# Performance work log

Measured on AMD Instinct MI355X. Metric: run time of the kernel, lower is better.

The kernel has to match this reference:

```python
import jax, jax.numpy as jnp
import numpy as np

B, T, FEAT, FUSION, H, C = 128, 64, 4096, 1024, 1024, 2


def setup_inputs() -> dict:
    key = jax.random.key(0)
    ks = jax.random.split(key, 9)
    s_feat = 1.0 / np.sqrt(FEAT)
    s_h = 1.0 / np.sqrt(H)
    return {
        "x": jax.random.normal(ks[0], (B, T, FEAT), jnp.float32),
        "W_feat": jax.random.normal(ks[1], (FUSION, FEAT), jnp.float32) * s_feat,
        "b_feat": jax.random.normal(ks[2], (FUSION,), jnp.float32) * s_feat,
        "W_ih": jax.random.normal(ks[3], (4 * H, FUSION), jnp.float32) * s_h,
        "b_ih": jax.random.normal(ks[4], (4 * H,), jnp.float32) * s_h,
        "W_hh": jax.random.normal(ks[5], (4 * H, H), jnp.float32) * s_h,
        "b_hh": jax.random.normal(ks[6], (4 * H,), jnp.float32) * s_h,
        "W_cls": jax.random.normal(ks[7], (C, H), jnp.float32) * s_h,
        "b_cls": jax.random.normal(ks[8], (C,), jnp.float32) * s_h,
    }


def reference(x, W_feat, b_feat, W_ih, b_ih, W_hh, b_hh, W_cls, b_cls):
    # x: [B, T, FEAT]. Sequential LSTMCell loop expressed as lax.scan over time.
    Hdim = W_hh.shape[1]
    Bb = x.shape[0]
    h0 = jnp.zeros((Bb, Hdim), x.dtype)
    c0 = jnp.zeros((Bb, Hdim), x.dtype)

    def step(carry, x_t):
        h, c = carry
        # feature extractor: Linear + ReLU fusion (dropout = identity in eval)
        f = jax.nn.relu(x_t @ W_feat.T + b_feat)  # [B, FUSION]
        gates = f @ W_ih.T + b_ih + h @ W_hh.T + b_hh  # [B, 4H]
        i, fg, g, o = jnp.split(gates, 4, axis=-1)  # torch LSTMCell gate order
        i = jax.nn.sigmoid(i)
        fg = jax.nn.sigmoid(fg)
        g = jnp.tanh(g)
        o = jax.nn.sigmoid(o)
        c_new = fg * c + i * g
        h_new = o * jnp.tanh(c_new)
        s = h_new @ W_cls.T + b_cls  # [B, 2]
        return (h_new, c_new), s

    xs = jnp.swapaxes(x, 0, 1)  # [T, B, FEAT]
    _, scores = jax.lax.scan(step, (h0, c0), xs)  # [T, B, 2]
    return jnp.swapaxes(scores, 0, 1)  # [B, T, 2]
```

## Files before the change

### kernel.cpp

```cpp
#include <hip/hip_runtime.h>
#include <math.h>


typedef __attribute__((ext_vector_type(8))) short short8v;
typedef __attribute__((ext_vector_type(4))) float f32x4;
typedef unsigned short u16;

#define HF2_BUF 262144
#define HF2_MT  32768

__device__ __forceinline__ short f2h(float f) {
    return __builtin_bit_cast(short, (_Float16)f);
}
__device__ __forceinline__ float h2f(u16 h) {
    return (float)__builtin_bit_cast(_Float16, (short)h);
}

__global__ void cvt_f16(const float* __restrict__ src, u16* __restrict__ d, int n4) {
    int i = blockIdx.x * blockDim.x + threadIdx.x;
    if (i >= n4) return;
    float4 v = ((const float4*)src)[i];
    ushort4 o;
    o.x = (u16)f2h(v.x); o.y = (u16)f2h(v.y);
    o.z = (u16)f2h(v.z); o.w = (u16)f2h(v.w);
    ((ushort4*)d)[i] = o;
}

template<bool A_PRE16, bool RELU, bool OUT_F16, bool OUT_GI>
__global__ __launch_bounds__(256)
void gemm_f16(const float* __restrict__ Af,
              const u16* __restrict__ A16, int lda,
              const u16* __restrict__ B16, int ldb,
              const float* __restrict__ bias,
              float* __restrict__ C, u16* __restrict__ C16,
              int ldc, int K)
{
    __shared__ short8v As[8][64];
    __shared__ short8v Bs[8][64];

    const int tid = threadIdx.x;
    const int l   = tid & 63;
    const int w   = tid >> 6;
    const int wm  = w & 1, wn = w >> 1;
    const int bm  = blockIdx.x * 128, bn = blockIdx.y * 128;

    const int sm    = tid >> 2;
    const int sk8   = (tid & 3) * 8;
    const int koct_s = sk8 >> 3;
    const int slane = ((sm & 15) ^ (koct_s << 1)) | (koct_s << 4);
    const int smf   = sm >> 4;
    const int lsw   = ((l & 15) ^ ((l >> 4) << 1)) | (l & 48);

    f32x4 acc[4][4];
#pragma unroll
    for (int i = 0; i < 4; ++i)
#pragma unroll
        for (int j = 0; j < 4; ++j)
#pragma unroll
            for (int r = 0; r < 4; ++r) acc[i][j][r] = 0.f;

    for (int k0 = 0; k0 < K; k0 += 32) {
        if constexpr (A_PRE16) {
            const size_t o0 = (size_t)(bm + sm) * lda + k0 + sk8;
            const size_t o1 = (size_t)(bm + sm + 64) * lda + k0 + sk8;
            As[smf][slane]     = *(const short8v*)(A16 + o0);
            As[smf + 4][slane] = *(const short8v*)(A16 + o1);
        } else {
            float fa[8], fb[8];
            const float* p0 = Af + (size_t)(bm + sm) * lda + k0 + sk8;
            const float* p1 = Af + (size_t)(bm + sm + 64) * lda + k0 + sk8;
            *(float4*)(fa)     = *(const float4*)(p0);
            *(float4*)(fa + 4) = *(const float4*)(p0 + 4);
            *(float4*)(fb)     = *(const float4*)(p1);
            *(float4*)(fb + 4) = *(const float4*)(p1 + 4);
            short8v ha, hb;
#pragma unroll
            for (int e = 0; e < 8; ++e) { ha[e] = f2h(fa[e]); hb[e] = f2h(fb[e]); }
            As[smf][slane]     = ha;
            As[smf + 4][slane] = hb;
        }
        {
            const size_t o0 = (size_t)(bn + sm) * ldb + k0 + sk8;
            const size_t o1 = (size_t)(bn + sm + 64) * ldb + k0 + sk8;
            Bs[smf][slane]     = *(const short8v*)(B16 + o0);
            Bs[smf + 4][slane] = *(const short8v*)(B16 + o1);
        }
        __syncthreads();

        short8v a[4];
#pragma unroll
        for (int i = 0; i < 4; ++i) a[i] = As[wm * 4 + i][lsw];
#pragma unroll
        for (int j = 0; j < 4; ++j) {
            const short8v b = Bs[wn * 4 + j][lsw];
#pragma unroll
            for (int i = 0; i < 4; ++i)
                acc[i][j] = __builtin_amdgcn_mfma_f32_16x16x32_f16(a[i], b, acc[i][j], 0, 0, 0);
        }
        __syncthreads();
    }

    const int row0 = bm + wm * 64 + (l >> 4) * 4;
    const int col0 = bn + wn * 64 + (l & 15);
#pragma unroll
    for (int i = 0; i < 4; ++i) {
#pragma unroll
        for (int j = 0; j < 4; ++j) {
            const int col = col0 + j * 16;
            const float bs = bias[col];
#pragma unroll
            for (int r = 0; r < 4; ++r) {
                const int row = row0 + i * 16 + r;
                float v = acc[i][j][r] + bs;
                if (RELU) v = fmaxf(v, 0.f);
                if (OUT_F16) {
                    C16[(size_t)row * ldc + col] = (u16)f2h(v);
                } else if (OUT_GI) {
                    const size_t rr = (size_t)(row & 63) * 128 + (row >> 6);
                    C16[rr * 4096 + (size_t)(col & 1023) * 4 + (col >> 10)] = (u16)f2h(v);
                } else {
                    C[(size_t)row * ldc + col] = v;
                }
            }
        }
    }
}

__global__ void pack_whh3(const float* __restrict__ W, char* __restrict__ Wf) {
    int gid = blockIdx.x * blockDim.x + threadIdx.x;
    int l = gid & 63, fid = gid >> 6;
    int kcl = fid & 15, kh = (fid >> 4) & 1, ngrp = (fid >> 5) & 63, g = fid >> 11;
    int n = g * 1024 + ngrp * 16 + (l & 15);
    int k = kh * 512 + kcl * 32 + (l >> 4) * 8;
    const float* src = W + (size_t)n * 1024 + k;
    short8v v16;
#pragma unroll
    for (int e = 0; e < 8; ++e) v16[e] = f2h(src[e]);
    *(short8v*)(Wf + (size_t)fid * 1024 + (size_t)l * 16) = v16;
}

__global__ void out_init(float* __restrict__ out, const float* __restrict__ b_cls) {
    int i = blockIdx.x * blockDim.x + threadIdx.x;
    if (i < 16384) out[i] = b_cls[i & 1];
}

__global__ __launch_bounds__(512)
void lstm_step(const u16* __restrict__ Gxi,
               const float* __restrict__ b_hh,
               const char*  __restrict__ Wf,
               char*        __restrict__ hfrag,
               float*       __restrict__ c,
               const float* __restrict__ Wc,
               float*       __restrict__ out,
               int t)
{
    __shared__ short8v Hs[64][64];
    __shared__ float gates_s[2][4][32][16];
    __shared__ float h_s[32][16];
    __shared__ float Wc_s[2][16];

    const int tid = threadIdx.x, bid = blockIdx.x;
    const int w = tid >> 6, l = tid & 63;
    const int g = w & 3, kh = w >> 2;
    const int ngrp = bid & 63, mh = bid >> 6;

    if (tid < 32) Wc_s[tid >> 4][tid & 15] =
        Wc[(size_t)(tid >> 4) * 1024 + ngrp * 16 + (tid & 15)];

    const int lhi = l >> 4;
    const int llo = l & 15;

    f32x4 aE0, aO0, aE1, aO1;
#pragma unroll
    for (int r = 0; r < 4; ++r) { aE0[r] = 0.f; aO0[r] = 0.f; aE1[r] = 0.f; aO1[r] = 0.f; }

    if (t > 0) {
        const char* hbase = hfrag + ((t - 1) & 1) * HF2_BUF;
#pragma unroll
        for (int it = 0; it < 8; ++it) {
            const int u  = tid + it * 512;
            const int s  = u >> 6;
            const int ln = u & 63;
            Hs[s][ln] = *(const short8v*)(hbase
                        + (size_t)(2 * mh + (s >> 5)) * HF2_MT
                        + (size_t)(s & 31) * 1024 + (size_t)ln * 16);
        }
        __syncthreads();

        const char* wb = Wf + (size_t)((g * 64 + ngrp) * 2 + kh) * 16384 + (size_t)l * 16;
#pragma unroll
        for (int kcl = 0; kcl < 16; kcl += 2) {
            const short8v b0 = *(const short8v*)(wb + kcl * 1024);
            const short8v b1 = *(const short8v*)(wb + (kcl + 1) * 1024);
            const int kc0 = kh * 16 + kcl;
            aE0 = __builtin_amdgcn_mfma_f32_16x16x32_f16(Hs[kc0][l],      b0, aE0, 0, 0, 0);
            aE1 = __builtin_amdgcn_mfma_f32_16x16x32_f16(Hs[32 + kc0][l], b0, aE1, 0, 0, 0);
            aO0 = __builtin_amdgcn_mfma_f32_16x16x32_f16(Hs[kc0 + 1][l],      b1, aO0, 0, 0, 0);
            aO1 = __builtin_amdgcn_mfma_f32_16x16x32_f16(Hs[32 + kc0 + 1][l], b1, aO1, 0, 0, 0);
        }
    }

#pragma unroll
    for (int r = 0; r < 4; ++r) {
        gates_s[kh][g][lhi * 4 + r][llo]      = aE0[r] + aO0[r];
        gates_s[kh][g][16 + lhi * 4 + r][llo] = aE1[r] + aO1[r];
    }
    __syncthreads();

    {
        const int r  = tid >> 4;
        const int cw = tid & 15;
        const int row = mh * 32 + r;
        const int col = ngrp * 16 + cw;
        const ushort4 gv = *(const ushort4*)(Gxi
                          + ((size_t)t * 128 + row) * 4096 + (size_t)col * 4);
        float gate[4];
        gate[0] = h2f(gv.x); gate[1] = h2f(gv.y);
        gate[2] = h2f(gv.z); gate[3] = h2f(gv.w);
#pragma unroll
        for (int gg = 0; gg < 4; ++gg)
            gate[gg] += gates_s[0][gg][r][cw] + gates_s[1][gg][r][cw]
                      + b_hh[gg * 1024 + col];
        float ig = 1.f / (1.f + __expf(-gate[0]));
        float fg = 1.f / (1.f + __expf(-gate[1]));
        float gg = tanhf(gate[2]);
        float og = 1.f / (1.f + __expf(-gate[3]));
        const size_t cidx = (size_t)row * 1024 + col;
        float cp = (t > 0) ? c[cidx] : 0.f;
        float cn = fg * cp + ig * gg;
        float hn = og * tanhf(cn);
        c[cidx] = cn;
        h_s[r][cw] = hn;

        float s0 = hn * Wc_s[0][cw];
        float s1 = hn * Wc_s[1][cw];
#pragma unroll
        for (int off = 8; off > 0; off >>= 1) {
            s0 += __shfl_xor(s0, off);
            s1 += __shfl_xor(s1, off);
        }
        if (cw == 0) {
            float* o = out + ((size_t)row * 64 + t) * 2;
            atomicAdd(o,     s0);
            atomicAdd(o + 1, s1);
        }
    }
    __syncthreads();

    if (tid < 64) {
        const int idx16  = tid & 15;
        const int koct_h = (tid >> 4) & 1;
        const int mt_l   = (tid >> 5) & 1;
        const int lane   = idx16 | (((ngrp & 1) * 2 + koct_h) << 4);
        short8v v;
#pragma unroll
        for (int e = 0; e < 8; ++e)
            v[e] = f2h(h_s[mt_l * 16 + idx16][koct_h * 8 + e]);
        char* dst = hfrag + (t & 1) * HF2_BUF
                  + (size_t)(2 * mh + mt_l) * HF2_MT
                  + (size_t)(ngrp >> 1) * 1024 + (size_t)lane * 16;
        *(short8v*)dst = v;
    }
}

extern "C" void kernel_launch(void* const* d_in, const int* in_sizes, int n_in,
                              void* d_out, int out_size, void* d_ws, size_t ws_size,
                              hipStream_t stream) {
    const float* x      = (const float*)d_in[0];
    const float* W_feat = (const float*)d_in[1];
    const float* b_feat = (const float*)d_in[2];
    const float* W_ih   = (const float*)d_in[3];
    const float* b_ih   = (const float*)d_in[4];
    const float* W_hh   = (const float*)d_in[5];
    const float* b_hh   = (const float*)d_in[6];
    const float* W_cls  = (const float*)d_in[7];
    const float* b_cls  = (const float*)d_in[8];
    float* out = (float*)d_out;

    char* ws = (char*)d_ws;
    u16*  F16   = (u16*)ws;
    u16*  Wih16 = (u16*)(ws + 16777216);
    u16*  Wf16  = (u16*)(ws + 25165824);
    u16*  Gxi   = (u16*)(ws + 33554432);
    char* Wf    = ws;
    char* hfrag = ws + 16777216;
    float* c    = (float*)(ws + 17825792);

    cvt_f16<<<dim3(4096), dim3(256), 0, stream>>>(W_feat, Wf16, 1048576);
    cvt_f16<<<dim3(4096), dim3(256), 0, stream>>>(W_ih, Wih16, 1048576);
    out_init<<<dim3(64), dim3(256), 0, stream>>>(out, b_cls);

    gemm_f16<false, true, true, false>
        <<<dim3(64, 8), 256, 0, stream>>>(
            x, nullptr, 4096, Wf16, 4096, b_feat,
            nullptr, F16, 1024, 4096);

    gemm_f16<true, false, false, true>
        <<<dim3(64, 32), 256, 0, stream>>>(
            nullptr, F16, 1024, Wih16, 1024, b_ih,
            nullptr, Gxi, 4096, 1024);

    pack_whh3<<<dim3(2048), dim3(256), 0, stream>>>(W_hh, Wf);

    for (int t = 0; t < 64; ++t) {
        lstm_step<<<dim3(256), dim3(512), 0, stream>>>(
            Gxi, b_hh, Wf, hfrag, c, W_cls, out, t);
    }
}
```

Measured before the change: 725.3 us.

## Fold b_hh into GEMM bias, prefetch gate inputs early, widen BK for feature GEMM

Adds a small kernel that pre-sums b_ih and b_hh so the input-projection GEMM bakes both biases into Gxi. This removes the per-step b_hh loads in the recurrent kernel. The Gxi gate values and previous cell state are now loaded at the start of lstm_step, so their latency overlaps the recurrent MFMA work. The feature GEMM also gets a templated K-tile of 64, which halves the number of barriers per K and doubles the LDS footprint.

```diff
diff --git a/kernel.cpp b/kernel.cpp
--- a/kernel.cpp
+++ b/kernel.cpp
@@ -26,7 +26,13 @@
     ((ushort4*)d)[i] = o;
 }
 
-template<bool A_PRE16, bool RELU, bool OUT_F16, bool OUT_GI>
+__global__ void add_bias(const float* __restrict__ a, const float* __restrict__ b,
+                         float* __restrict__ o, int n) {
+    int i = blockIdx.x * blockDim.x + threadIdx.x;
+    if (i < n) o[i] = a[i] + b[i];
+}
+
+template<int BK, bool A_PRE16, bool RELU, bool OUT_F16, bool OUT_GI>
 __global__ __launch_bounds__(256)
 void gemm_f16(const float* __restrict__ Af,
               const u16* __restrict__ A16, int lda,
@@ -35,8 +41,9 @@
               float* __restrict__ C, u16* __restrict__ C16,
               int ldc, int K)
 {
-    __shared__ short8v As[8][64];
-    __shared__ short8v Bs[8][64];
+    constexpr int NH = BK / 32;
+    __shared__ short8v As[NH * 8][64];
+    __shared__ short8v Bs[NH * 8][64];
 
     const int tid = threadIdx.x;
     const int l   = tid & 63;
@@ -59,43 +66,44 @@
 #pragma unroll
             for (int r = 0; r < 4; ++r) acc[i][j][r] = 0.f;
 
-    for (int k0 = 0; k0 < K; k0 += 32) {
-        if constexpr (A_PRE16) {
-            const size_t o0 = (size_t)(bm + sm) * lda + k0 + sk8;
-            const size_t o1 = (size_t)(bm + sm + 64) * lda + k0 + sk8;
-            As[smf][slane]     = *(const short8v*)(A16 + o0);
-            As[smf + 4][slane] = *(const short8v*)(A16 + o1);
-        } else {
-            float fa[8], fb[8];
-            const float* p0 = Af + (size_t)(bm + sm) * lda + k0 + sk8;
-            const float* p1 = Af + (size_t)(bm + sm + 64) * lda + k0 + sk8;
-            *(float4*)(fa)     = *(const float4*)(p0);
-            *(float4*)(fa + 4) = *(const float4*)(p0 + 4);
-            *(float4*)(fb)     = *(const float4*)(p1);
-            *(float4*)(fb + 4) = *(const float4*)(p1 + 4);
-            short8v ha, hb;
-#pragma unroll
-            for (int e = 0; e < 8; ++e) { ha[e] = f2h(fa[e]); hb[e] = f2h(fb[e]); }
-            As[smf][slane]     = ha;
-            As[smf + 4][slane] = hb;
-        }
-        {
-            const size_t o0 = (size_t)(bn + sm) * ldb + k0 + sk8;
-            const size_t o1 = (size_t)(bn + sm + 64) * ldb + k0 + sk8;
-            Bs[smf][slane]     = *(const short8v*)(B16 + o0);
-            Bs[smf + 4][slane] = *(const short8v*)(B16 + o1);
+    for (int k0 = 0; k0 < K; k0 += BK) {
+#pragma unroll
+        for (int h = 0; h < NH; ++h) {
+            const int kk = k0 + h * 32 + sk8;
+            if constexpr (A_PRE16) {
+                As[h * 8 + smf][slane]     = *(const short8v*)(A16 + (size_t)(bm + sm) * lda + kk);
+                As[h * 8 + smf + 4][slane] = *(const short8v*)(A16 + (size_t)(bm + sm + 64) * lda + kk);
+            } else {
+                float fa[8], fb[8];
+                const float* p0 = Af + (size_t)(bm + sm) * lda + kk;
+                const float* p1 = Af + (size_t)(bm + sm + 64) * lda + kk;
+                *(float4*)(fa)     = *(const float4*)(p0);
+                *(float4*)(fa + 4) = *(const float4*)(p0 + 4);
+                *(float4*)(fb)     = *(const float4*)(p1);
+                *(float4*)(fb + 4) = *(const float4*)(p1 + 4);
+                short8v ha, hb;
+#pragma unroll
+                for (int e = 0; e < 8; ++e) { ha[e] = f2h(fa[e]); hb[e] = f2h(fb[e]); }
+                As[h * 8 + smf][slane]     = ha;
+                As[h * 8 + smf + 4][slane] = hb;
+            }
+            Bs[h * 8 + smf][slane]     = *(const short8v*)(B16 + (size_t)(bn + sm) * ldb + kk);
+            Bs[h * 8 + smf + 4][slane] = *(const short8v*)(B16 + (size_t)(bn + sm + 64) * ldb + kk);
         }
         __syncthreads();
 
-        short8v a[4];
-#pragma unroll
-        for (int i = 0; i < 4; ++i) a[i] = As[wm * 4 + i][lsw];
-#pragma unroll
-        for (int j = 0; j < 4; ++j) {
-            const short8v b = Bs[wn * 4 + j][lsw];
-#pragma unroll
-            for (int i = 0; i < 4; ++i)
-                acc[i][j] = __builtin_amdgcn_mfma_f32_16x16x32_f16(a[i], b, acc[i][j], 0, 0, 0);
+#pragma unroll
+        for (int h = 0; h < NH; ++h) {
+            short8v a[4];
+#pragma unroll
+            for (int i = 0; i < 4; ++i) a[i] = As[h * 8 + wm * 4 + i][lsw];
+#pragma unroll
+            for (int j = 0; j < 4; ++j) {
+                const short8v b = Bs[h * 8 + wn * 4 + j][lsw];
+#pragma unroll
+                for (int i = 0; i < 4; ++i)
+                    acc[i][j] = __builtin_amdgcn_mfma_f32_16x16x32_f16(a[i], b, acc[i][j], 0, 0, 0);
+            }
         }
         __syncthreads();
     }
@@ -146,7 +154,6 @@
 
 __global__ __launch_bounds__(512)
 void lstm_step(const u16* __restrict__ Gxi,
-               const float* __restrict__ b_hh,
                const char*  __restrict__ Wf,
                char*        __restrict__ hfrag,
                float*       __restrict__ c,
@@ -164,6 +171,15 @@
     const int g = w & 3, kh = w >> 2;
     const int ngrp = bid & 63, mh = bid >> 6;
 
+    const int r_c  = tid >> 4;
+    const int cw_c = tid & 15;
+    const int row_c = mh * 32 + r_c;
+    const int col_c = ngrp * 16 + cw_c;
+    const ushort4 gv = *(const ushort4*)(Gxi
+                      + ((size_t)t * 128 + row_c) * 4096 + (size_t)col_c * 4);
+    const size_t cidx = (size_t)row_c * 1024 + col_c;
+    const float cp = (t > 0) ? c[cidx] : 0.f;
+
     if (tid < 32) Wc_s[tid >> 4][tid & 15] =
         Wc[(size_t)(tid >> 4) * 1024 + ngrp * 16 + (tid & 15)];
 
@@ -208,39 +224,30 @@
     __syncthreads();
 
     {
-        const int r  = tid >> 4;
-        const int cw = tid & 15;
-        const int row = mh * 32 + r;
-        const int col = ngrp * 16 + cw;
-        const ushort4 gv = *(const ushort4*)(Gxi
-                          + ((size_t)t * 128 + row) * 4096 + (size_t)col * 4);
         float gate[4];
         gate[0] = h2f(gv.x); gate[1] = h2f(gv.y);
         gate[2] = h2f(gv.z); gate[3] = h2f(gv.w);
 #pragma unroll
         for (int gg = 0; gg < 4; ++gg)
-            gate[gg] += gates_s[0][gg][r][cw] + gates_s[1][gg][r][cw]
-                      + b_hh[gg * 1024 + col];
+            gate[gg] += gates_s[0][gg][r_c][cw_c] + gates_s[1][gg][r_c][cw_c];
         float ig = 1.f / (1.f + __expf(-gate[0]));
         float fg = 1.f / (1.f + __expf(-gate[1]));
         float gg = tanhf(gate[2]);
         float og = 1.f / (1.f + __expf(-gate[3]));
-        const size_t cidx = (size_t)row * 1024 + col;
-        float cp = (t > 0) ? c[cidx] : 0.f;
         float cn = fg * cp + ig * gg;
         float hn = og * tanhf(cn);
         c[cidx] = cn;
-        h_s[r][cw] = hn;
-
-        float s0 = hn * Wc_s[0][cw];
-        float s1 = hn * Wc_s[1][cw];
+        h_s[r_c][cw_c] = hn;
+
+        float s0 = hn * Wc_s[0][cw_c];
+        float s1 = hn * Wc_s[1][cw_c];
 #pragma unroll
         for (int off = 8; off > 0; off >>= 1) {
             s0 += __shfl_xor(s0, off);
             s1 += __shfl_xor(s1, off);
         }
-        if (cw == 0) {
-            float* o = out + ((size_t)row * 64 + t) * 2;
+        if (cw_c == 0) {
+            float* o = out + ((size_t)row_c * 64 + t) * 2;
             atomicAdd(o,     s0);
             atomicAdd(o + 1, s1);
         }
@@ -282,28 +289,30 @@
     u16*  Wih16 = (u16*)(ws + 16777216);
     u16*  Wf16  = (u16*)(ws + 25165824);
     u16*  Gxi   = (u16*)(ws + 33554432);
+    float* bsum = (float*)(ws + 104857600);
     char* Wf    = ws;
     char* hfrag = ws + 16777216;
     float* c    = (float*)(ws + 17825792);
 
     cvt_f16<<<dim3(4096), dim3(256), 0, stream>>>(W_feat, Wf16, 1048576);
     cvt_f16<<<dim3(4096), dim3(256), 0, stream>>>(W_ih, Wih16, 1048576);
+    add_bias<<<dim3(16), dim3(256), 0, stream>>>(b_ih, b_hh, bsum, 4096);
     out_init<<<dim3(64), dim3(256), 0, stream>>>(out, b_cls);
 
-    gemm_f16<false, true, true, false>
+    gemm_f16<64, false, true, true, false>
         <<<dim3(64, 8), 256, 0, stream>>>(
             x, nullptr, 4096, Wf16, 4096, b_feat,
             nullptr, F16, 1024, 4096);
 
-    gemm_f16<true, false, false, true>
+    gemm_f16<32, true, false, false, true>
         <<<dim3(64, 32), 256, 0, stream>>>(
-            nullptr, F16, 1024, Wih16, 1024, b_ih,
+            nullptr, F16, 1024, Wih16, 1024, bsum,
             nullptr, Gxi, 4096, 1024);
 
     pack_whh3<<<dim3(2048), dim3(256), 0, stream>>>(W_hh, Wf);
 
     for (int t = 0; t < 64; ++t) {
         lstm_step<<<dim3(256), dim3(512), 0, stream>>>(
-            Gxi, b_hh, Wf, hfrag, c, W_cls, out, t);
-    }
-}
+            Gxi, Wf, hfrag, c, W_cls, out, t);
+    }
+}
```

New measurement: 683.0 us. 1.06x faster.
